# Optimization experiments

Measured on AMD Instinct MI355X. Metric: run time of the kernel, lower is better.

Reference implementation:

```python
import jax, jax.numpy as jnp
import numpy as np
import math

EPS = 1e-5      # artanh boundary clamp (Poincare ball)
MIN_NORM = 1e-15

def _norm(x):
    return jnp.clip(jnp.linalg.norm(x, axis=-1, keepdims=True), MIN_NORM, None)

def artanh(x):
    x = jnp.clip(x, -1.0 + EPS, 1.0 - EPS)
    return 0.5 * (jnp.log1p(x) - jnp.log1p(-x))

def expmap0(u):
    # c = 1 Poincare ball: tanh(||u||) * u / ||u||
    n = _norm(u)
    return jnp.tanh(n) * u / n

def mobius_matvec(M, x):
    # geoopt: mx = x @ M^T; res = tanh(||mx||/||x|| * artanh(||x||)) * mx/||mx||
    xn = _norm(x)
    mx = x @ M.T
    mxn = _norm(mx)
    res = jnp.tanh(mxn / xn * artanh(xn)) * mx / mxn
    zero_row = jnp.all(mx == 0, axis=-1, keepdims=True)
    return jnp.where(zero_row, jnp.zeros_like(res), res)

def mobius_add(x, y):
    x2 = jnp.sum(x * x, axis=-1, keepdims=True)
    y2 = jnp.sum(y * y, axis=-1, keepdims=True)
    xy = jnp.sum(x * y, axis=-1, keepdims=True)
    num = (1.0 + 2.0 * xy + y2) * x + (1.0 - x2) * y
    den = 1.0 + 2.0 * xy + x2 * y2
    return num / jnp.clip(den, MIN_NORM, None)

def dist(x, y):
    # d(x,y) = 2 * artanh(|| (-x) mobius+ y ||); reduces the last dim
    return 2.0 * artanh(_norm(mobius_add(-x, y)))[..., 0]

def setup_inputs() -> dict:
    key = jax.random.key(0)
    k1, k2, k3, k4, k5 = jax.random.split(key, 5)
    B, S, H, D = 64, 1024, 768, 64
    bound = 1.0 / math.sqrt(D)
    sequence_output = jax.random.normal(k1, (B, S, H), dtype=jnp.float32) * 0.1
    proj = jax.random.uniform(k2, (H, D), dtype=jnp.float32, minval=-0.05, maxval=0.05)
    trans = jax.random.uniform(k3, (D, D), dtype=jnp.float32, minval=-0.05, maxval=0.05)
    pos = expmap0(jax.random.uniform(k4, (D,), dtype=jnp.float32, minval=-bound, maxval=bound))
    neg = expmap0(jax.random.uniform(k5, (D,), dtype=jnp.float32, minval=-bound, maxval=bound))
    return {"sequence_output": sequence_output, "proj": proj, "trans": trans,
            "pos": pos, "neg": neg}

def reference(sequence_output, proj, trans, pos, neg):
    t = sequence_output @ proj          # [B, S, 64]
    t = expmap0(t)
    t = mobius_matvec(trans, t)
    pos_logits = dist(neg, t).sum(-1)   # [B]
    neg_logits = dist(pos, t).sum(-1)   # [B]
    return jnp.stack((neg_logits, pos_logits), axis=-1)  # [B, 2]
```

## Files before the change

### kernel.cpp

```cpp
#include <hip/hip_runtime.h>
#include <math.h>

#define MIN_NORM 1e-15f
#define BOUND_EPS 1e-5f

typedef __attribute__((ext_vector_type(8))) short short8v;
typedef __attribute__((ext_vector_type(4))) float f32x4;

__device__ __forceinline__ unsigned short f2bf(float f) {
  unsigned int u = __float_as_uint(f);
  unsigned int r = (u + 0x7FFFu + ((u >> 16) & 1u)) >> 16;
  return (unsigned short)r;
}

__device__ __forceinline__ float gred16(float v) {
  v += __shfl_xor(v, 1, 64);
  v += __shfl_xor(v, 2, 64);
  v += __shfl_xor(v, 4, 64);
  v += __shfl_xor(v, 8, 64);
  return v;
}
__device__ __forceinline__ float wred64(float v) {
#pragma unroll
  for (int off = 32; off; off >>= 1) v += __shfl_xor(v, off, 64);
  return v;
}
__device__ __forceinline__ float artanh_c(float x) {
  x = fminf(fmaxf(x, -1.f + BOUND_EPS), 1.f - BOUND_EPS);
  return 0.5f * logf((1.f + x) / (1.f - x));
}

__global__ __launch_bounds__(256) void poincare_prep(
    const float* __restrict__ proj, const float* __restrict__ trans,
    unsigned short* __restrict__ projB, unsigned short* __restrict__ transB) {
  int idx = blockIdx.x * 256 + threadIdx.x;
  if (idx < 49152) {
    int k = idx >> 6, d = idx & 63;
    int kt = k >> 5, t5 = k & 31, lk = t5 >> 3, j = t5 & 7;
    int nt = d >> 4, lr = d & 15;
    int l = lk * 16 + lr;
    projB[((kt * 4 + nt) * 64 + l) * 8 + j] = f2bf(proj[idx]);
  } else if (idx < 49152 + 4096) {
    int i2 = idx - 49152;
    int r = i2 >> 6, c = i2 & 63;
    int nt = r >> 4, lr = r & 15;
    int kt = c >> 5, lk = (c >> 3) & 3, j = c & 7;
    int l = lk * 16 + lr;
    transB[((kt * 4 + nt) * 64 + l) * 8 + j] = f2bf(trans[i2]);
  }
}

__global__ __launch_bounds__(512, 4) void poincare_main(
    const float* __restrict__ seq,
    const unsigned short* __restrict__ projB,
    const unsigned short* __restrict__ transB,
    const float* __restrict__ pos, const float* __restrict__ neg,
    float* __restrict__ wsPart) {
  __shared__ unsigned short teL[4][16 * 64];
  __shared__ float xbuf[4][64][17];
  __shared__ float partial[4][2];

  const int tid = threadIdx.x;
  const int w = tid >> 6, l = tid & 63;
  const int p = w & 3, h = w >> 2;
  const int lr = l & 15, lk = l >> 4;
  const long bIdx = blockIdx.x;

  const float* pA = seq + ((bIdx * 64 + p * 16 + lr) * 768 + h * 384 + lk * 8);
  const unsigned short* pB = projB + h * 12 * 2048 + l * 8;

  f32x4 acc[4];
#pragma unroll
  for (int nt = 0; nt < 4; ++nt) acc[nt] = (f32x4){0.f, 0.f, 0.f, 0.f};

  for (int kt = 0; kt < 12; kt += 4) {
    float4 a[8];
#pragma unroll
    for (int u = 0; u < 4; ++u) {
      a[2 * u]     = *(const float4*)(pA + 32 * u);
      a[2 * u + 1] = *(const float4*)(pA + 32 * u + 4);
    }
    pA += 128;
#pragma unroll
    for (int u = 0; u < 4; ++u) {
      const unsigned short* pb = pB + (kt + u) * 2048;
      short8v b0 = *(const short8v*)(pb);
      short8v b1 = *(const short8v*)(pb + 512);
      short8v b2 = *(const short8v*)(pb + 1024);
      short8v b3 = *(const short8v*)(pb + 1536);
      short8v av;
      av[0] = (short)f2bf(a[2 * u].x); av[1] = (short)f2bf(a[2 * u].y);
      av[2] = (short)f2bf(a[2 * u].z); av[3] = (short)f2bf(a[2 * u].w);
      av[4] = (short)f2bf(a[2 * u + 1].x); av[5] = (short)f2bf(a[2 * u + 1].y);
      av[6] = (short)f2bf(a[2 * u + 1].z); av[7] = (short)f2bf(a[2 * u + 1].w);
      acc[0] = __builtin_amdgcn_mfma_f32_16x16x32_bf16(av, b0, acc[0], 0, 0, 0);
      acc[1] = __builtin_amdgcn_mfma_f32_16x16x32_bf16(av, b1, acc[1], 0, 0, 0);
      acc[2] = __builtin_amdgcn_mfma_f32_16x16x32_bf16(av, b2, acc[2], 0, 0, 0);
      acc[3] = __builtin_amdgcn_mfma_f32_16x16x32_bf16(av, b3, acc[3], 0, 0, 0);
    }
  }

  if (h) {
#pragma unroll
    for (int nt = 0; nt < 4; ++nt)
#pragma unroll
      for (int i = 0; i < 4; ++i) xbuf[p][l][nt * 4 + i] = acc[nt][i];
  }
  __syncthreads();

  float th[4];
  if (!h) {
#pragma unroll
    for (int nt = 0; nt < 4; ++nt)
#pragma unroll
      for (int i = 0; i < 4; ++i) acc[nt][i] += xbuf[p][l][nt * 4 + i];

#pragma unroll
    for (int i = 0; i < 4; ++i) {
      float s = acc[0][i] * acc[0][i] + acc[1][i] * acc[1][i] +
                acc[2][i] * acc[2][i] + acc[3][i] * acc[3][i];
      s = gred16(s);
      float n = fmaxf(sqrtf(s), MIN_NORM);
      float t = tanhf(n);
      th[i] = fmaxf(t, MIN_NORM);
      float sc = t / n;
#pragma unroll
      for (int nt = 0; nt < 4; ++nt) acc[nt][i] *= sc;
    }

    unsigned short* buf = teL[p];
#pragma unroll
    for (int i = 0; i < 4; ++i) {
      int row = lk * 4 + i;
      int sw = (row & 7) << 3;
#pragma unroll
      for (int nt = 0; nt < 4; ++nt) {
        int col = nt * 16 + lr;
        buf[row * 64 + (col ^ sw)] = f2bf(acc[nt][i]);
      }
    }
  }
  __syncthreads();

  if (!h) {
    const unsigned short* buf = teL[p];
    f32x4 acc2[4];
#pragma unroll
    for (int nt = 0; nt < 4; ++nt) acc2[nt] = (f32x4){0.f, 0.f, 0.f, 0.f};
    const unsigned short* pT = transB + l * 8;
#pragma unroll
    for (int kt = 0; kt < 2; ++kt) {
      short8v a2 = *(const short8v*)&buf[lr * 64 + ((kt * 32 + lk * 8) ^ ((lr & 7) << 3))];
      const unsigned short* pt = pT + kt * 2048;
      short8v c0 = *(const short8v*)(pt);
      short8v c1 = *(const short8v*)(pt + 512);
      short8v c2 = *(const short8v*)(pt + 1024);
      short8v c3 = *(const short8v*)(pt + 1536);
      acc2[0] = __builtin_amdgcn_mfma_f32_16x16x32_bf16(a2, c0, acc2[0], 0, 0, 0);
      acc2[1] = __builtin_amdgcn_mfma_f32_16x16x32_bf16(a2, c1, acc2[1], 0, 0, 0);
      acc2[2] = __builtin_amdgcn_mfma_f32_16x16x32_bf16(a2, c2, acc2[2], 0, 0, 0);
      acc2[3] = __builtin_amdgcn_mfma_f32_16x16x32_bf16(a2, c3, acc2[3], 0, 0, 0);
    }

    float xp[4], xq[4];
#pragma unroll
    for (int nt = 0; nt < 4; ++nt) {
      xp[nt] = pos[nt * 16 + lr];
      xq[nt] = neg[nt * 16 + lr];
    }
    float x2p = wred64(xp[0] * xp[0] + xp[1] * xp[1] + xp[2] * xp[2] + xp[3] * xp[3]) * 0.25f;
    float x2n = wred64(xq[0] * xq[0] + xq[1] * xq[1] + xq[2] * xq[2] + xq[3] * xq[3]) * 0.25f;

    float distP = 0.f, distN = 0.f;
#pragma unroll
    for (int i = 0; i < 4; ++i) {
      float m0 = acc2[0][i], m1 = acc2[1][i], m2 = acc2[2][i], m3 = acc2[3][i];
      float s = gred16(m0 * m0 + m1 * m1 + m2 * m2 + m3 * m3);
      float mxn = fmaxf(sqrtf(s), MIN_NORM);
      float xn = th[i];
      float rs = tanhf(mxn / xn * artanh_c(xn)) / mxn;
      float r0 = rs * m0, r1 = rs * m1, r2 = rs * m2, r3 = rs * m3;
      float y2 = gred16(r0 * r0 + r1 * r1 + r2 * r2 + r3 * r3);
      float xyP = -gred16(xp[0] * r0 + xp[1] * r1 + xp[2] * r2 + xp[3] * r3);
      float xyN = -gred16(xq[0] * r0 + xq[1] * r1 + xq[2] * r2 + xq[3] * r3);
      {
        float A = 1.f + 2.f * xyP + y2, B = 1.f - x2p;
        float inv = 1.f / fmaxf(1.f + 2.f * xyP + x2p * y2, MIN_NORM);
        float v0 = (B * r0 - A * xp[0]) * inv, v1 = (B * r1 - A * xp[1]) * inv;
        float v2 = (B * r2 - A * xp[2]) * inv, v3 = (B * r3 - A * xp[3]) * inv;
        float nv = fmaxf(sqrtf(gred16(v0 * v0 + v1 * v1 + v2 * v2 + v3 * v3)), MIN_NORM);
        distP += 2.f * artanh_c(nv);
      }
      {
        float A = 1.f + 2.f * xyN + y2, B = 1.f - x2n;
        float inv = 1.f / fmaxf(1.f + 2.f * xyN + x2n * y2, MIN_NORM);
        float v0 = (B * r0 - A * xq[0]) * inv, v1 = (B * r1 - A * xq[1]) * inv;
        float v2 = (B * r2 - A * xq[2]) * inv, v3 = (B * r3 - A * xq[3]) * inv;
        float nv = fmaxf(sqrtf(gred16(v0 * v0 + v1 * v1 + v2 * v2 + v3 * v3)), MIN_NORM);
        distN += 2.f * artanh_c(nv);
      }
    }
    float tP = wred64(distP) * 0.0625f;
    float tN = wred64(distN) * 0.0625f;
    if (l == 0) { partial[p][0] = tP; partial[p][1] = tN; }
  }
  __syncthreads();
  if (tid == 0) {
    wsPart[0 * 1024 + bIdx] = partial[0][0] + partial[1][0] + partial[2][0] + partial[3][0];
    wsPart[1 * 1024 + bIdx] = partial[0][1] + partial[1][1] + partial[2][1] + partial[3][1];
  }
}

__global__ __launch_bounds__(128) void poincare_reduce(const float* __restrict__ wsPart,
                                                       float* __restrict__ out) {
  int t = threadIdx.x;
  int b = t >> 1, j = t & 1;
  const float4* v = (const float4*)(wsPart + j * 1024 + b * 16);
  float s = 0.f;
#pragma unroll
  for (int i = 0; i < 4; ++i) s += v[i].x + v[i].y + v[i].z + v[i].w;
  out[b * 2 + j] = s;
}

extern "C" void kernel_launch(void* const* d_in, const int* in_sizes, int n_in,
                              void* d_out, int out_size, void* d_ws, size_t ws_size,
                              hipStream_t stream) {
  const float* seq = (const float*)d_in[0];
  const float* proj = (const float*)d_in[1];
  const float* trans = (const float*)d_in[2];
  const float* pos = (const float*)d_in[3];
  const float* neg = (const float*)d_in[4];

  unsigned short* projB = (unsigned short*)d_ws;
  unsigned short* transB = projB + 49152;
  float* wsPart = (float*)((char*)d_ws + 106496);
  float* out = (float*)d_out;

  poincare_prep<<<208, 256, 0, stream>>>(proj, trans, projB, transB);
  poincare_main<<<1024, 512, 0, stream>>>(seq, projB, transB, pos, neg, wsPart);
  poincare_reduce<<<1, 128, 0, stream>>>(wsPart, out);
}
```

Measured before the change: 55.09 us.

## Stage sequence tiles through double-buffered LDS with 4-wave blocks, dropping split-K

The main kernel now uses 256 threads per block instead of 512. The K dimension is no longer split across two wave groups, so the LDS reduction buffer for the split halves goes away. Each 64x128 chunk of the fp32 input is loaded with coalesced float4 reads, converted to bf16 and written into a padded double buffer in LDS. The next chunk is prefetched into registers while MFMAs run on the current one. The aim is better coalescing and overlap of global loads with compute, at the cost of fewer waves per block, more LDS and a barrier per chunk.

```diff
diff --git a/kernel.cpp b/kernel.cpp
--- a/kernel.cpp
+++ b/kernel.cpp
@@ -11,6 +11,9 @@
   unsigned int u = __float_as_uint(f);
   unsigned int r = (u + 0x7FFFu + ((u >> 16) & 1u)) >> 16;
   return (unsigned short)r;
+}
+__device__ __forceinline__ unsigned int pack2bf(float a, float b) {
+  return (unsigned int)f2bf(a) | ((unsigned int)f2bf(b) << 16);
 }
 
 __device__ __forceinline__ float gred16(float v) {
@@ -50,160 +53,166 @@
   }
 }
 
-__global__ __launch_bounds__(512, 4) void poincare_main(
+__global__ __launch_bounds__(256, 3) void poincare_main(
     const float* __restrict__ seq,
     const unsigned short* __restrict__ projB,
     const unsigned short* __restrict__ transB,
     const float* __restrict__ pos, const float* __restrict__ neg,
     float* __restrict__ wsPart) {
+  __shared__ unsigned short As[2][64][136];
   __shared__ unsigned short teL[4][16 * 64];
-  __shared__ float xbuf[4][64][17];
   __shared__ float partial[4][2];
 
   const int tid = threadIdx.x;
   const int w = tid >> 6, l = tid & 63;
-  const int p = w & 3, h = w >> 2;
   const int lr = l & 15, lk = l >> 4;
   const long bIdx = blockIdx.x;
-
-  const float* pA = seq + ((bIdx * 64 + p * 16 + lr) * 768 + h * 384 + lk * 8);
-  const unsigned short* pB = projB + h * 12 * 2048 + l * 8;
+  const float* sBase = seq + bIdx * 64 * 768;
+
+  const int rS = tid >> 5;
+  const int cS = (tid & 31) * 4;
 
   f32x4 acc[4];
 #pragma unroll
   for (int nt = 0; nt < 4; ++nt) acc[nt] = (f32x4){0.f, 0.f, 0.f, 0.f};
 
-  for (int kt = 0; kt < 12; kt += 4) {
-    float4 a[8];
-#pragma unroll
-    for (int u = 0; u < 4; ++u) {
-      a[2 * u]     = *(const float4*)(pA + 32 * u);
-      a[2 * u + 1] = *(const float4*)(pA + 32 * u + 4);
-    }
-    pA += 128;
-#pragma unroll
-    for (int u = 0; u < 4; ++u) {
-      const unsigned short* pb = pB + (kt + u) * 2048;
-      short8v b0 = *(const short8v*)(pb);
-      short8v b1 = *(const short8v*)(pb + 512);
-      short8v b2 = *(const short8v*)(pb + 1024);
-      short8v b3 = *(const short8v*)(pb + 1536);
-      short8v av;
-      av[0] = (short)f2bf(a[2 * u].x); av[1] = (short)f2bf(a[2 * u].y);
-      av[2] = (short)f2bf(a[2 * u].z); av[3] = (short)f2bf(a[2 * u].w);
-      av[4] = (short)f2bf(a[2 * u + 1].x); av[5] = (short)f2bf(a[2 * u + 1].y);
-      av[6] = (short)f2bf(a[2 * u + 1].z); av[7] = (short)f2bf(a[2 * u + 1].w);
-      acc[0] = __builtin_amdgcn_mfma_f32_16x16x32_bf16(av, b0, acc[0], 0, 0, 0);
-      acc[1] = __builtin_amdgcn_mfma_f32_16x16x32_bf16(av, b1, acc[1], 0, 0, 0);
-      acc[2] = __builtin_amdgcn_mfma_f32_16x16x32_bf16(av, b2, acc[2], 0, 0, 0);
-      acc[3] = __builtin_amdgcn_mfma_f32_16x16x32_bf16(av, b3, acc[3], 0, 0, 0);
-    }
-  }
-
-  if (h) {
-#pragma unroll
-    for (int nt = 0; nt < 4; ++nt)
-#pragma unroll
-      for (int i = 0; i < 4; ++i) xbuf[p][l][nt * 4 + i] = acc[nt][i];
+#pragma unroll
+  for (int i = 0; i < 8; ++i) {
+    int r = i * 8 + rS;
+    float4 v = *(const float4*)(sBase + r * 768 + cS);
+    *(uint2*)&As[0][r][cS] = make_uint2(pack2bf(v.x, v.y), pack2bf(v.z, v.w));
   }
   __syncthreads();
 
+#pragma unroll 2
+  for (int ch = 0; ch < 6; ++ch) {
+    const int cur = ch & 1;
+
+    short8v bf[4][4];
+#pragma unroll
+    for (int ktl = 0; ktl < 4; ++ktl) {
+      const unsigned short* pb = projB + (ch * 4 + ktl) * 2048 + l * 8;
+      bf[ktl][0] = *(const short8v*)(pb);
+      bf[ktl][1] = *(const short8v*)(pb + 512);
+      bf[ktl][2] = *(const short8v*)(pb + 1024);
+      bf[ktl][3] = *(const short8v*)(pb + 1536);
+    }
+
+    float4 st[8];
+    if (ch < 5) {
+#pragma unroll
+      for (int i = 0; i < 8; ++i) {
+        int r = i * 8 + rS;
+        st[i] = *(const float4*)(sBase + r * 768 + (ch + 1) * 128 + cS);
+      }
+    }
+
+#pragma unroll
+    for (int ktl = 0; ktl < 4; ++ktl) {
+      short8v av = *(const short8v*)&As[cur][w * 16 + lr][ktl * 32 + lk * 8];
+      acc[0] = __builtin_amdgcn_mfma_f32_16x16x32_bf16(av, bf[ktl][0], acc[0], 0, 0, 0);
+      acc[1] = __builtin_amdgcn_mfma_f32_16x16x32_bf16(av, bf[ktl][1], acc[1], 0, 0, 0);
+      acc[2] = __builtin_amdgcn_mfma_f32_16x16x32_bf16(av, bf[ktl][2], acc[2], 0, 0, 0);
+      acc[3] = __builtin_amdgcn_mfma_f32_16x16x32_bf16(av, bf[ktl][3], acc[3], 0, 0, 0);
+    }
+
+    if (ch < 5) {
+#pragma unroll
+      for (int i = 0; i < 8; ++i) {
+        int r = i * 8 + rS;
+        *(uint2*)&As[cur ^ 1][r][cS] =
+            make_uint2(pack2bf(st[i].x, st[i].y), pack2bf(st[i].z, st[i].w));
+      }
+    }
+    __syncthreads();
+  }
+
   float th[4];
-  if (!h) {
-#pragma unroll
-    for (int nt = 0; nt < 4; ++nt)
-#pragma unroll
-      for (int i = 0; i < 4; ++i) acc[nt][i] += xbuf[p][l][nt * 4 + i];
-
-#pragma unroll
-    for (int i = 0; i < 4; ++i) {
-      float s = acc[0][i] * acc[0][i] + acc[1][i] * acc[1][i] +
-                acc[2][i] * acc[2][i] + acc[3][i] * acc[3][i];
-      s = gred16(s);
-      float n = fmaxf(sqrtf(s), MIN_NORM);
-      float t = tanhf(n);
-      th[i] = fmaxf(t, MIN_NORM);
-      float sc = t / n;
-#pragma unroll
-      for (int nt = 0; nt < 4; ++nt) acc[nt][i] *= sc;
-    }
-
-    unsigned short* buf = teL[p];
-#pragma unroll
-    for (int i = 0; i < 4; ++i) {
-      int row = lk * 4 + i;
-      int sw = (row & 7) << 3;
-#pragma unroll
-      for (int nt = 0; nt < 4; ++nt) {
-        int col = nt * 16 + lr;
-        buf[row * 64 + (col ^ sw)] = f2bf(acc[nt][i]);
-      }
+#pragma unroll
+  for (int i = 0; i < 4; ++i) {
+    float s = acc[0][i] * acc[0][i] + acc[1][i] * acc[1][i] +
+              acc[2][i] * acc[2][i] + acc[3][i] * acc[3][i];
+    s = gred16(s);
+    float n = fmaxf(sqrtf(s), MIN_NORM);
+    float t = tanhf(n);
+    th[i] = fmaxf(t, MIN_NORM);
+    float sc = t / n;
+#pragma unroll
+    for (int nt = 0; nt < 4; ++nt) acc[nt][i] *= sc;
+  }
+
+  unsigned short* buf = teL[w];
+#pragma unroll
+  for (int i = 0; i < 4; ++i) {
+    int row = lk * 4 + i;
+    int sw = (row & 7) << 3;
+#pragma unroll
+    for (int nt = 0; nt < 4; ++nt) {
+      int col = nt * 16 + lr;
+      buf[row * 64 + (col ^ sw)] = f2bf(acc[nt][i]);
     }
   }
   __syncthreads();
 
-  if (!h) {
-    const unsigned short* buf = teL[p];
-    f32x4 acc2[4];
-#pragma unroll
-    for (int nt = 0; nt < 4; ++nt) acc2[nt] = (f32x4){0.f, 0.f, 0.f, 0.f};
-    const unsigned short* pT = transB + l * 8;
-#pragma unroll
-    for (int kt = 0; kt < 2; ++kt) {
-      short8v a2 = *(const short8v*)&buf[lr * 64 + ((kt * 32 + lk * 8) ^ ((lr & 7) << 3))];
-      const unsigned short* pt = pT + kt * 2048;
-      short8v c0 = *(const short8v*)(pt);
-      short8v c1 = *(const short8v*)(pt + 512);
-      short8v c2 = *(const short8v*)(pt + 1024);
-      short8v c3 = *(const short8v*)(pt + 1536);
-      acc2[0] = __builtin_amdgcn_mfma_f32_16x16x32_bf16(a2, c0, acc2[0], 0, 0, 0);
-      acc2[1] = __builtin_amdgcn_mfma_f32_16x16x32_bf16(a2, c1, acc2[1], 0, 0, 0);
-      acc2[2] = __builtin_amdgcn_mfma_f32_16x16x32_bf16(a2, c2, acc2[2], 0, 0, 0);
-      acc2[3] = __builtin_amdgcn_mfma_f32_16x16x32_bf16(a2, c3, acc2[3], 0, 0, 0);
-    }
-
-    float xp[4], xq[4];
-#pragma unroll
-    for (int nt = 0; nt < 4; ++nt) {
-      xp[nt] = pos[nt * 16 + lr];
-      xq[nt] = neg[nt * 16 + lr];
-    }
-    float x2p = wred64(xp[0] * xp[0] + xp[1] * xp[1] + xp[2] * xp[2] + xp[3] * xp[3]) * 0.25f;
-    float x2n = wred64(xq[0] * xq[0] + xq[1] * xq[1] + xq[2] * xq[2] + xq[3] * xq[3]) * 0.25f;
-
-    float distP = 0.f, distN = 0.f;
-#pragma unroll
-    for (int i = 0; i < 4; ++i) {
-      float m0 = acc2[0][i], m1 = acc2[1][i], m2 = acc2[2][i], m3 = acc2[3][i];
-      float s = gred16(m0 * m0 + m1 * m1 + m2 * m2 + m3 * m3);
-      float mxn = fmaxf(sqrtf(s), MIN_NORM);
-      float xn = th[i];
-      float rs = tanhf(mxn / xn * artanh_c(xn)) / mxn;
-      float r0 = rs * m0, r1 = rs * m1, r2 = rs * m2, r3 = rs * m3;
-      float y2 = gred16(r0 * r0 + r1 * r1 + r2 * r2 + r3 * r3);
-      float xyP = -gred16(xp[0] * r0 + xp[1] * r1 + xp[2] * r2 + xp[3] * r3);
-      float xyN = -gred16(xq[0] * r0 + xq[1] * r1 + xq[2] * r2 + xq[3] * r3);
-      {
-        float A = 1.f + 2.f * xyP + y2, B = 1.f - x2p;
-        float inv = 1.f / fmaxf(1.f + 2.f * xyP + x2p * y2, MIN_NORM);
-        float v0 = (B * r0 - A * xp[0]) * inv, v1 = (B * r1 - A * xp[1]) * inv;
-        float v2 = (B * r2 - A * xp[2]) * inv, v3 = (B * r3 - A * xp[3]) * inv;
-        float nv = fmaxf(sqrtf(gred16(v0 * v0 + v1 * v1 + v2 * v2 + v3 * v3)), MIN_NORM);
-        distP += 2.f * artanh_c(nv);
-      }
-      {
-        float A = 1.f + 2.f * xyN + y2, B = 1.f - x2n;
-        float inv = 1.f / fmaxf(1.f + 2.f * xyN + x2n * y2, MIN_NORM);
-        float v0 = (B * r0 - A * xq[0]) * inv, v1 = (B * r1 - A * xq[1]) * inv;
-        float v2 = (B * r2 - A * xq[2]) * inv, v3 = (B * r3 - A * xq[3]) * inv;
-        float nv = fmaxf(sqrtf(gred16(v0 * v0 + v1 * v1 + v2 * v2 + v3 * v3)), MIN_NORM);
-        distN += 2.f * artanh_c(nv);
-      }
-    }
-    float tP = wred64(distP) * 0.0625f;
-    float tN = wred64(distN) * 0.0625f;
-    if (l == 0) { partial[p][0] = tP; partial[p][1] = tN; }
-  }
+  f32x4 acc2[4];
+#pragma unroll
+  for (int nt = 0; nt < 4; ++nt) acc2[nt] = (f32x4){0.f, 0.f, 0.f, 0.f};
+  const unsigned short* pT = transB + l * 8;
+#pragma unroll
+  for (int kt = 0; kt < 2; ++kt) {
+    short8v a2 = *(const short8v*)&buf[lr * 64 + ((kt * 32 + lk * 8) ^ ((lr & 7) << 3))];
+    const unsigned short* pt = pT + kt * 2048;
+    short8v c0 = *(const short8v*)(pt);
+    short8v c1 = *(const short8v*)(pt + 512);
+    short8v c2 = *(const short8v*)(pt + 1024);
+    short8v c3 = *(const short8v*)(pt + 1536);
+    acc2[0] = __builtin_amdgcn_mfma_f32_16x16x32_bf16(a2, c0, acc2[0], 0, 0, 0);
+    acc2[1] = __builtin_amdgcn_mfma_f32_16x16x32_bf16(a2, c1, acc2[1], 0, 0, 0);
+    acc2[2] = __builtin_amdgcn_mfma_f32_16x16x32_bf16(a2, c2, acc2[2], 0, 0, 0);
+    acc2[3] = __builtin_amdgcn_mfma_f32_16x16x32_bf16(a2, c3, acc2[3], 0, 0, 0);
+  }
+
+  float xp[4], xq[4];
+#pragma unroll
+  for (int nt = 0; nt < 4; ++nt) {
+    xp[nt] = pos[nt * 16 + lr];
+    xq[nt] = neg[nt * 16 + lr];
+  }
+  float x2p = wred64(xp[0] * xp[0] + xp[1] * xp[1] + xp[2] * xp[2] + xp[3] * xp[3]) * 0.25f;
+  float x2n = wred64(xq[0] * xq[0] + xq[1] * xq[1] + xq[2] * xq[2] + xq[3] * xq[3]) * 0.25f;
+
+  float distP = 0.f, distN = 0.f;
+#pragma unroll
+  for (int i = 0; i < 4; ++i) {
+    float m0 = acc2[0][i], m1 = acc2[1][i], m2 = acc2[2][i], m3 = acc2[3][i];
+    float s = gred16(m0 * m0 + m1 * m1 + m2 * m2 + m3 * m3);
+    float mxn = fmaxf(sqrtf(s), MIN_NORM);
+    float xn = th[i];
+    float rs = tanhf(mxn / xn * artanh_c(xn)) / mxn;
+    float r0 = rs * m0, r1 = rs * m1, r2 = rs * m2, r3 = rs * m3;
+    float y2 = gred16(r0 * r0 + r1 * r1 + r2 * r2 + r3 * r3);
+    float xyP = -gred16(xp[0] * r0 + xp[1] * r1 + xp[2] * r2 + xp[3] * r3);
+    float xyN = -gred16(xq[0] * r0 + xq[1] * r1 + xq[2] * r2 + xq[3] * r3);
+    {
+      float A = 1.f + 2.f * xyP + y2, B = 1.f - x2p;
+      float inv = 1.f / fmaxf(1.f + 2.f * xyP + x2p * y2, MIN_NORM);
+      float v0 = (B * r0 - A * xp[0]) * inv, v1 = (B * r1 - A * xp[1]) * inv;
+      float v2 = (B * r2 - A * xp[2]) * inv, v3 = (B * r3 - A * xp[3]) * inv;
+      float nv = fmaxf(sqrtf(gred16(v0 * v0 + v1 * v1 + v2 * v2 + v3 * v3)), MIN_NORM);
+      distP += 2.f * artanh_c(nv);
+    }
+    {
+      float A = 1.f + 2.f * xyN + y2, B = 1.f - x2n;
+      float inv = 1.f / fmaxf(1.f + 2.f * xyN + x2n * y2, MIN_NORM);
+      float v0 = (B * r0 - A * xq[0]) * inv, v1 = (B * r1 - A * xq[1]) * inv;
+      float v2 = (B * r2 - A * xq[2]) * inv, v3 = (B * r3 - A * xq[3]) * inv;
+      float nv = fmaxf(sqrtf(gred16(v0 * v0 + v1 * v1 + v2 * v2 + v3 * v3)), MIN_NORM);
+      distN += 2.f * artanh_c(nv);
+    }
+  }
+  float tP = wred64(distP) * 0.0625f;
+  float tN = wred64(distN) * 0.0625f;
+  if (l == 0) { partial[w][0] = tP; partial[w][1] = tN; }
   __syncthreads();
   if (tid == 0) {
     wsPart[0 * 1024 + bIdx] = partial[0][0] + partial[1][0] + partial[2][0] + partial[3][0];
@@ -237,6 +246,6 @@
   float* out = (float*)d_out;
 
   poincare_prep<<<208, 256, 0, stream>>>(proj, trans, projB, transB);
-  poincare_main<<<1024, 512, 0, stream>>>(seq, projB, transB, pos, neg, wsPart);
+  poincare_main<<<1024, 256, 0, stream>>>(seq, projB, transB, pos, neg, wsPart);
   poincare_reduce<<<1, 128, 0, stream>>>(wsPart, out);
 }
```

Measured after the change: 51.06 us. 7.3% less time.
